# Optimization experiments

Measured on AMD Instinct MI355X. Metric: run time of the kernel, lower is better.

The kernel has to match this reference:

```python
import jax, jax.numpy as jnp
import numpy as np

B, T, IN, H, OUT = 16384, 60, 1, 50, 1


def setup_inputs() -> dict:
    key = jax.random.key(0)
    ks = jax.random.split(key, 7)
    s = 1.0 / np.sqrt(H)
    return {
        "input_seq": jax.random.normal(ks[0], (B, T, IN), dtype=jnp.float32),
        "w_ih": jax.random.uniform(ks[1], (4 * H, IN), jnp.float32, -s, s),
        "w_hh": jax.random.uniform(ks[2], (4 * H, H), jnp.float32, -s, s),
        "b_ih": jax.random.uniform(ks[3], (4 * H,), jnp.float32, -s, s),
        "b_hh": jax.random.uniform(ks[4], (4 * H,), jnp.float32, -s, s),
        "w_lin": jax.random.uniform(ks[5], (OUT, H * T), jnp.float32, -s, s),
        "b_lin": jax.random.uniform(ks[6], (OUT,), jnp.float32, -s, s),
    }


def reference(input_seq, w_ih, w_hh, b_ih, b_hh, w_lin, b_lin):
    # Precompute input projections for all timesteps: [T, B, 4H]
    x_proj = jnp.einsum('bti,gi->tbg', input_seq, w_ih) + b_ih + b_hh

    def step(carry, xp):
        h, c = carry
        gates = xp + h @ w_hh.T  # [B, 4H]
        i, f, g, o = jnp.split(gates, 4, axis=-1)  # PyTorch gate order
        i, f, o = jax.nn.sigmoid(i), jax.nn.sigmoid(f), jax.nn.sigmoid(o)
        g = jnp.tanh(g)
        c = f * c + i * g
        h = o * jnp.tanh(c)
        return (h, c), h

    h0 = jnp.zeros((input_seq.shape[0], H), dtype=input_seq.dtype)
    (_, _), hs = jax.lax.scan(step, (h0, h0), x_proj)  # hs: [T, B, H]
    lstm_out = jnp.transpose(hs, (1, 0, 2)).reshape(-1, H * T)  # [B, T*H]
    return lstm_out @ w_lin.T + b_lin
```

## Files before the change

### kernel.cpp

```cpp
#include <hip/hip_runtime.h>


namespace {
constexpr int TS = 60;

typedef _Float16 half8 __attribute__((ext_vector_type(8)));
typedef _Float16 half2v __attribute__((ext_vector_type(2)));
typedef float f32x4 __attribute__((ext_vector_type(4)));

__device__ __forceinline__ float fexp2(float x) { return __builtin_amdgcn_exp2f(x); }
__device__ __forceinline__ float frcp(float x) { return __builtin_amdgcn_rcpf(x); }
__device__ __forceinline__ f32x4 mfma16(half8 a, half8 b, f32x4 c) {
  return __builtin_amdgcn_mfma_f32_16x16x32_f16(a, b, c, 0, 0, 0);
}
}

__global__ __launch_bounds__(64, 1) void lstm_wv(
    const float* __restrict__ x,
    const float* __restrict__ w_ih,
    const float* __restrict__ w_hh,
    const float* __restrict__ b_ih,
    const float* __restrict__ b_hh,
    const float* __restrict__ w_lin,
    const float* __restrict__ b_lin,
    float* __restrict__ out)
{
  __shared__ unsigned HB[2][16 * 32];
  __shared__ float WLT[4 * 13 * 60];
  __shared__ float XL[TS * 16];

  const int lane = threadIdx.x;
  const int g = lane >> 4;
  const int cl = lane & 15;
  const int s8 = cl & 7;
  const long bbase = (long)blockIdx.x * 16;

  for (int i = lane; i < TS * 16; i += 64) {
    const int b = i / TS, t = i - b * TS;
    XL[t * 16 + b] = x[bbase * TS + i];
  }
  for (int i = lane; i < 4 * 13 * TS; i += 64) {
    const int gg = i / (13 * TS), rem = i - gg * (13 * TS);
    const int T = rem / TS, t = rem - T * TS;
    const int u = 4 * T + gg;
    WLT[i] = (u < 50) ? w_lin[t * 50 + u] : 0.0f;
  }
  for (int i = lane; i < 1024; i += 64) ((unsigned*)HB)[i] = 0u;

  half8 A[13][2];
  {
    const int gate = cl & 3, ur = cl >> 2;
#pragma unroll
    for (int T = 0; T < 13; ++T) {
      const int uA = 4 * T + ur;
      const int orig = gate * 50 + uA;
      const bool valid = (uA < 50);
#pragma unroll
      for (int kc = 0; kc < 2; ++kc) {
        half8 frag;
#pragma unroll
        for (int e = 0; e < 8; ++e) {
          const int k = kc * 32 + 8 * g + e;
          const int j = k >> 3, s = (k >> 1) & 3, cb = k & 1;
          float v = 0.0f;
          if (valid) {
            if (j <= 6) {
              const int u = 8 * j + 4 * cb + s;
              if (u < 50) v = w_hh[orig * 50 + u];
            } else if (k == 62) {
              v = b_ih[orig] + b_hh[orig];
            } else if (k == 63) {
              v = w_ih[orig];
            }
          }
          frag[e] = (_Float16)v;
        }
        A[T][kc] = frag;
      }
    }
  }

  asm volatile("s_waitcnt lgkmcnt(0)" ::: "memory");
  __builtin_amdgcn_sched_barrier(0);

  const int rowb = cl * 32;
  const int clg = rowb + g;
  if (g == 3) {
    const half2v sp = {(_Float16)1.0f, (_Float16)XL[cl]};
    HB[0][clg + ((7 ^ s8) << 2)] = __builtin_bit_cast(unsigned, sp);
  }

  const unsigned b0off = rowb + ((g ^ s8) << 2);
  const unsigned b1off = rowb + (((4 | g) ^ s8) << 2);
  const float* wlb = &WLT[g * 13 * TS];

  float c[13];
#pragma unroll
  for (int T = 0; T < 13; ++T) c[T] = 0.0f;
  float oacc = 0.0f;

  constexpr float L1 = 1.4426950408889634f;
  constexpr float L2 = 2.8853901817779268f;

#pragma unroll 1
  for (int t = 0; t < TS; ++t) {
    const unsigned* HR = HB[t & 1];
    unsigned* HW = HB[(t & 1) ^ 1];
    const half8 B0 = *(const half8*)&HR[b0off];
    const half8 B1 = *(const half8*)&HR[b1off];

    f32x4 d[13];
#pragma unroll
    for (int T = 0; T < 13; ++T) {
      f32x4 a = {0.f, 0.f, 0.f, 0.f};
      a = mfma16(A[T][0], B0, a);
      a = mfma16(A[T][1], B1, a);
      d[T] = a;
    }

    _Float16 hh[14];
    hh[13] = (_Float16)0.0f;
#pragma unroll
    for (int T = 0; T < 13; ++T) {
      const float E1 = fexp2(-L1 * d[T][0]);
      const float E2 = fexp2(-L1 * d[T][1]);
      const float E3 = fexp2(-L1 * d[T][3]);
      const float E4 = fexp2(L2 * d[T][2]);
      const float P1 = 1.0f + E1, P2 = 1.0f + E2;
      const float P3 = 1.0f + E3, P4 = 1.0f + E4;
      const float p12 = P1 * P2, p34 = P3 * P4;
      const float r = frcp(p12 * p34);
      const float r12 = r * p34, r34 = r * p12;
      const float si = r12 * P2, sf = r12 * P1;
      const float so = r34 * P4;
      const float tg = fmaf(-2.0f, r34 * P3, 1.0f);
      const float cn = fmaf(sf, c[T], si * tg);
      c[T] = cn;
      const float Ec = fexp2(L2 * cn);
      const float tc = fmaf(-2.0f, frcp(1.0f + Ec), 1.0f);
      const float hn = so * tc;
      oacc = fmaf(hn, wlb[T * TS + t], oacc);
      hh[T] = (_Float16)hn;
    }

#pragma unroll
    for (int j = 0; j < 7; ++j) {
      const half2v hp = {hh[2 * j], hh[2 * j + 1]};
      HW[clg + ((j ^ s8) << 2)] = __builtin_bit_cast(unsigned, hp);
    }
    if (g == 3) {
      const int tn = (t + 1 < TS) ? (t + 1) : (TS - 1);
      const half2v sp = {(_Float16)1.0f, (_Float16)XL[tn * 16 + cl]};
      HW[clg + ((7 ^ s8) << 2)] = __builtin_bit_cast(unsigned, sp);
    }
    asm volatile("s_waitcnt lgkmcnt(0)" ::: "memory");
    __builtin_amdgcn_sched_barrier(0);
  }

  oacc += __shfl_xor(oacc, 32);
  oacc += __shfl_xor(oacc, 16);
  if (lane < 16) out[bbase + lane] = oacc + b_lin[0];
}

extern "C" void kernel_launch(void* const* d_in, const int* in_sizes, int n_in,
                              void* d_out, int out_size, void* d_ws, size_t ws_size,
                              hipStream_t stream) {
  const float* x     = (const float*)d_in[0];
  const float* w_ih  = (const float*)d_in[1];
  const float* w_hh  = (const float*)d_in[2];
  const float* b_ih  = (const float*)d_in[3];
  const float* b_hh  = (const float*)d_in[4];
  const float* w_lin = (const float*)d_in[5];
  const float* b_lin = (const float*)d_in[6];
  float* out = (float*)d_out;

  dim3 grid(16384 / 16);
  dim3 block(64);
  lstm_wv<<<grid, block, 0, stream>>>(x, w_ih, w_hh, b_ih, b_hh, w_lin,
                                      b_lin, out);
}
```

Measured before the change: 108.1 us.

## Split LSTM hidden units across 8 waves per block with shared h exchange

Replaces the one-wave-per-16-sequences design with 512-thread blocks in which 8 waves each own 2 hidden-unit tiles. Each block handles 32 sequences as two groups. The h state is exchanged through LDS with a __syncthreads every timestep, and partial outputs are reduced across waves at the end. This shortens the serial per-timestep chain for each wave (4 MFMA tiles instead of 13) and raises occupancy, at the cost of a block-wide barrier per step and fewer blocks in the grid. The hidden-unit mapping and the LDS swizzle were redone to match. The L2 constant was also slightly altered, which looks like a typo.

```diff
diff --git a/kernel.cpp b/kernel.cpp
--- a/kernel.cpp
+++ b/kernel.cpp
@@ -7,6 +7,7 @@
 typedef _Float16 half8 __attribute__((ext_vector_type(8)));
 typedef _Float16 half2v __attribute__((ext_vector_type(2)));
 typedef float f32x4 __attribute__((ext_vector_type(4)));
+typedef float f32x2 __attribute__((ext_vector_type(2)));
 
 __device__ __forceinline__ float fexp2(float x) { return __builtin_amdgcn_exp2f(x); }
 __device__ __forceinline__ float frcp(float x) { return __builtin_amdgcn_rcpf(x); }
@@ -15,7 +16,7 @@
 }
 }
 
-__global__ __launch_bounds__(64, 1) void lstm_wv(
+__global__ __launch_bounds__(512, 4) void lstm_w8x2(
     const float* __restrict__ x,
     const float* __restrict__ w_ih,
     const float* __restrict__ w_hh,
@@ -25,34 +26,36 @@
     const float* __restrict__ b_lin,
     float* __restrict__ out)
 {
-  __shared__ unsigned HB[2][16 * 32];
-  __shared__ float WLT[4 * 13 * 60];
-  __shared__ float XL[TS * 16];
+  __shared__ unsigned Hs[2][2][512];
+  __shared__ float WL[TS * 64];
+  __shared__ float XL[TS * 32];
+  __shared__ float OB[8][2][16];
 
-  const int lane = threadIdx.x;
+  const int tid = threadIdx.x;
+  const int lane = tid & 63;
+  const int wv = tid >> 6;
   const int g = lane >> 4;
   const int cl = lane & 15;
   const int s8 = cl & 7;
-  const long bbase = (long)blockIdx.x * 16;
+  const long bbase = (long)blockIdx.x * 32;
 
-  for (int i = lane; i < TS * 16; i += 64) {
+  for (int i = tid; i < TS * 32; i += 512) {
     const int b = i / TS, t = i - b * TS;
-    XL[t * 16 + b] = x[bbase * TS + i];
+    XL[t * 32 + b] = x[bbase * TS + i];
   }
-  for (int i = lane; i < 4 * 13 * TS; i += 64) {
-    const int gg = i / (13 * TS), rem = i - gg * (13 * TS);
-    const int T = rem / TS, t = rem - T * TS;
-    const int u = 4 * T + gg;
-    WLT[i] = (u < 50) ? w_lin[t * 50 + u] : 0.0f;
+  for (int i = tid; i < TS * 64; i += 512) {
+    const int t = i >> 6, u = i & 63;
+    WL[i] = (u < 50) ? w_lin[t * 50 + u] : 0.0f;
   }
-  for (int i = lane; i < 1024; i += 64) ((unsigned*)HB)[i] = 0u;
+  for (int i = tid; i < 2048; i += 512) ((unsigned*)Hs)[i] = 0u;
 
-  half8 A[13][2];
+  half8 A[2][2];
   {
     const int gate = cl & 3, ur = cl >> 2;
 #pragma unroll
-    for (int T = 0; T < 13; ++T) {
-      const int uA = 4 * T + ur;
+    for (int tau = 0; tau < 2; ++tau) {
+      const int T = 2 * wv + tau;
+      const int uA = 16 * ur + T;
       const int orig = gate * 50 + uA;
       const bool valid = (uA < 50);
 #pragma unroll
@@ -61,105 +64,119 @@
 #pragma unroll
         for (int e = 0; e < 8; ++e) {
           const int k = kc * 32 + 8 * g + e;
-          const int j = k >> 3, s = (k >> 1) & 3, cb = k & 1;
           float v = 0.0f;
           if (valid) {
-            if (j <= 6) {
-              const int u = 8 * j + 4 * cb + s;
-              if (u < 50) v = w_hh[orig * 50 + u];
-            } else if (k == 62) {
-              v = b_ih[orig] + b_hh[orig];
-            } else if (k == 63) {
-              v = w_ih[orig];
-            }
+            if (k < 50) v = w_hh[orig * 50 + k];
+            else if (k == 62) v = b_ih[orig] + b_hh[orig];
+            else if (k == 63) v = w_ih[orig];
           }
           frag[e] = (_Float16)v;
         }
-        A[T][kc] = frag;
+        A[tau][kc] = frag;
       }
     }
   }
+  __syncthreads();
 
-  asm volatile("s_waitcnt lgkmcnt(0)" ::: "memory");
-  __builtin_amdgcn_sched_barrier(0);
+  if (wv == 7 && g == 3) {
+#pragma unroll
+    for (int grp = 0; grp < 2; ++grp) {
+      const half2v sp = {(_Float16)1.0f, (_Float16)XL[grp * 16 + cl]};
+      Hs[grp][0][cl * 32 + (((7 ^ s8) << 2) | 3)] =
+          __builtin_bit_cast(unsigned, sp);
+    }
+  }
+  __syncthreads();
 
-  const int rowb = cl * 32;
-  const int clg = rowb + g;
-  if (g == 3) {
-    const half2v sp = {(_Float16)1.0f, (_Float16)XL[cl]};
-    HB[0][clg + ((7 ^ s8) << 2)] = __builtin_bit_cast(unsigned, sp);
-  }
+  const int rowdw = cl * 32;
+  const int rd0 = rowdw + ((g ^ s8) << 2);
+  const int rd1 = rowdw + (((4 | g) ^ s8) << 2);
+  const int hw = 16 * g + 2 * wv;
+  const int wd = rowdw + ((((hw >> 3) ^ s8) << 2) | ((hw & 7) >> 1));
 
-  const unsigned b0off = rowb + ((g ^ s8) << 2);
-  const unsigned b1off = rowb + (((4 | g) ^ s8) << 2);
-  const float* wlb = &WLT[g * 13 * TS];
-
-  float c[13];
-#pragma unroll
-  for (int T = 0; T < 13; ++T) c[T] = 0.0f;
-  float oacc = 0.0f;
+  float c[2][2] = {{0.f, 0.f}, {0.f, 0.f}};
+  float oacc[2] = {0.f, 0.f};
 
   constexpr float L1 = 1.4426950408889634f;
-  constexpr float L2 = 2.8853901817779268f;
+  constexpr float L2 = 2.8853900817779268f;
 
 #pragma unroll 1
   for (int t = 0; t < TS; ++t) {
-    const unsigned* HR = HB[t & 1];
-    unsigned* HW = HB[(t & 1) ^ 1];
-    const half8 B0 = *(const half8*)&HR[b0off];
-    const half8 B1 = *(const half8*)&HR[b1off];
+    const int p = t & 1;
+    half8 B0[2], B1[2];
+#pragma unroll
+    for (int grp = 0; grp < 2; ++grp) {
+      B0[grp] = *(const half8*)&Hs[grp][p][rd0];
+      B1[grp] = *(const half8*)&Hs[grp][p][rd1];
+    }
+    f32x4 d[2][2];
+#pragma unroll
+    for (int grp = 0; grp < 2; ++grp) {
+#pragma unroll
+      for (int tau = 0; tau < 2; ++tau) {
+        f32x4 a = {0.f, 0.f, 0.f, 0.f};
+        a = mfma16(A[tau][0], B0[grp], a);
+        a = mfma16(A[tau][1], B1[grp], a);
+        d[grp][tau] = a;
+      }
+    }
+    const f32x2 wl = *(const f32x2*)&WL[t * 64 + hw];
 
-    f32x4 d[13];
+    half2v hh[2];
 #pragma unroll
-    for (int T = 0; T < 13; ++T) {
-      f32x4 a = {0.f, 0.f, 0.f, 0.f};
-      a = mfma16(A[T][0], B0, a);
-      a = mfma16(A[T][1], B1, a);
-      d[T] = a;
+    for (int grp = 0; grp < 2; ++grp) {
+#pragma unroll
+      for (int tau = 0; tau < 2; ++tau) {
+        const float E1 = fexp2(-L1 * d[grp][tau][0]);
+        const float E2 = fexp2(-L1 * d[grp][tau][1]);
+        const float E3 = fexp2(-L1 * d[grp][tau][3]);
+        const float E4 = fexp2(L2 * d[grp][tau][2]);
+        const float P1 = 1.0f + E1, P2 = 1.0f + E2;
+        const float P3 = 1.0f + E3, P4 = 1.0f + E4;
+        const float p12 = P1 * P2, p34 = P3 * P4;
+        const float r = frcp(p12 * p34);
+        const float r12 = r * p34, r34 = r * p12;
+        const float si = r12 * P2, sf = r12 * P1;
+        const float so = r34 * P4;
+        const float tg = fmaf(-2.0f, r34 * P3, 1.0f);
+        const float cn = fmaf(sf, c[grp][tau], si * tg);
+        c[grp][tau] = cn;
+        const float Ec = fexp2(L2 * cn);
+        const float tc = fmaf(-2.0f, frcp(1.0f + Ec), 1.0f);
+        const float hn = so * tc;
+        oacc[grp] = fmaf(hn, wl[tau], oacc[grp]);
+        hh[grp][tau] = (_Float16)hn;
+      }
     }
 
-    _Float16 hh[14];
-    hh[13] = (_Float16)0.0f;
-#pragma unroll
-    for (int T = 0; T < 13; ++T) {
-      const float E1 = fexp2(-L1 * d[T][0]);
-      const float E2 = fexp2(-L1 * d[T][1]);
-      const float E3 = fexp2(-L1 * d[T][3]);
-      const float E4 = fexp2(L2 * d[T][2]);
-      const float P1 = 1.0f + E1, P2 = 1.0f + E2;
-      const float P3 = 1.0f + E3, P4 = 1.0f + E4;
-      const float p12 = P1 * P2, p34 = P3 * P4;
-      const float r = frcp(p12 * p34);
-      const float r12 = r * p34, r34 = r * p12;
-      const float si = r12 * P2, sf = r12 * P1;
-      const float so = r34 * P4;
-      const float tg = fmaf(-2.0f, r34 * P3, 1.0f);
-      const float cn = fmaf(sf, c[T], si * tg);
-      c[T] = cn;
-      const float Ec = fexp2(L2 * cn);
-      const float tc = fmaf(-2.0f, frcp(1.0f + Ec), 1.0f);
-      const float hn = so * tc;
-      oacc = fmaf(hn, wlb[T * TS + t], oacc);
-      hh[T] = (_Float16)hn;
+    if (wv == 7 && g == 3) {
+      const int tn = (t + 1 < TS) ? (t + 1) : (TS - 1);
+      hh[0][0] = (_Float16)1.0f;
+      hh[0][1] = (_Float16)XL[tn * 32 + cl];
+      hh[1][0] = (_Float16)1.0f;
+      hh[1][1] = (_Float16)XL[tn * 32 + 16 + cl];
     }
-
-#pragma unroll
-    for (int j = 0; j < 7; ++j) {
-      const half2v hp = {hh[2 * j], hh[2 * j + 1]};
-      HW[clg + ((j ^ s8) << 2)] = __builtin_bit_cast(unsigned, hp);
-    }
-    if (g == 3) {
-      const int tn = (t + 1 < TS) ? (t + 1) : (TS - 1);
-      const half2v sp = {(_Float16)1.0f, (_Float16)XL[tn * 16 + cl]};
-      HW[clg + ((7 ^ s8) << 2)] = __builtin_bit_cast(unsigned, sp);
-    }
-    asm volatile("s_waitcnt lgkmcnt(0)" ::: "memory");
-    __builtin_amdgcn_sched_barrier(0);
+    Hs[0][p ^ 1][wd] = __builtin_bit_cast(unsigned, hh[0]);
+    Hs[1][p ^ 1][wd] = __builtin_bit_cast(unsigned, hh[1]);
+    __syncthreads();
   }
 
-  oacc += __shfl_xor(oacc, 32);
-  oacc += __shfl_xor(oacc, 16);
-  if (lane < 16) out[bbase + lane] = oacc + b_lin[0];
+  oacc[0] += __shfl_xor(oacc[0], 32);
+  oacc[0] += __shfl_xor(oacc[0], 16);
+  oacc[1] += __shfl_xor(oacc[1], 32);
+  oacc[1] += __shfl_xor(oacc[1], 16);
+  if (lane < 16) {
+    OB[wv][0][cl] = oacc[0];
+    OB[wv][1][cl] = oacc[1];
+  }
+  __syncthreads();
+  if (tid < 32) {
+    const int grp = tid >> 4, b = tid & 15;
+    float s = b_lin[0];
+#pragma unroll
+    for (int q = 0; q < 8; ++q) s += OB[q][grp][b];
+    out[bbase + grp * 16 + b] = s;
+  }
 }
 
 extern "C" void kernel_launch(void* const* d_in, const int* in_sizes, int n_in,
@@ -174,8 +191,8 @@
   const float* b_lin = (const float*)d_in[6];
   float* out = (float*)d_out;
 
-  dim3 grid(16384 / 16);
-  dim3 block(64);
-  lstm_wv<<<grid, block, 0, stream>>>(x, w_ih, w_hh, b_ih, b_hh, w_lin,
-                                      b_lin, out);
+  dim3 grid(16384 / 32);
+  dim3 block(512);
+  lstm_w8x2<<<grid, block, 0, stream>>>(x, w_ih, w_hh, b_ih, b_hh, w_lin,
+                                        b_lin, out);
 }
```

After: 99.78 us. 1.08x faster.

## Keep LSTM hidden state in registers by remapping gate rows to MFMA layout

Applied to the files above, without the earlier changes.

Reorders the weight-fragment row mapping so that the MFMA output layout of h directly matches the B-operand layout for the next timestep. This removes the per-step LDS write/read double buffer and its wait. The output projection weights are restaged per timestep and read with vector loads. In exchange, the padding grows from 13 to 16 tiles, adding MFMA and transcendental work per step, and a constant was slightly altered.

```diff
diff --git a/kernel.cpp b/kernel.cpp
--- a/kernel.cpp
+++ b/kernel.cpp
@@ -5,7 +5,6 @@
 constexpr int TS = 60;
 
 typedef _Float16 half8 __attribute__((ext_vector_type(8)));
-typedef _Float16 half2v __attribute__((ext_vector_type(2)));
 typedef float f32x4 __attribute__((ext_vector_type(4)));
 
 __device__ __forceinline__ float fexp2(float x) { return __builtin_amdgcn_exp2f(x); }
@@ -15,7 +14,7 @@
 }
 }
 
-__global__ __launch_bounds__(64, 1) void lstm_wv(
+__global__ __launch_bounds__(64, 1) void lstm_reg(
     const float* __restrict__ x,
     const float* __restrict__ w_ih,
     const float* __restrict__ w_hh,
@@ -25,136 +24,121 @@
     const float* __restrict__ b_lin,
     float* __restrict__ out)
 {
-  __shared__ unsigned HB[2][16 * 32];
-  __shared__ float WLT[4 * 13 * 60];
+  __shared__ float WL[TS * 64];
   __shared__ float XL[TS * 16];
 
   const int lane = threadIdx.x;
   const int g = lane >> 4;
   const int cl = lane & 15;
-  const int s8 = cl & 7;
   const long bbase = (long)blockIdx.x * 16;
 
   for (int i = lane; i < TS * 16; i += 64) {
     const int b = i / TS, t = i - b * TS;
     XL[t * 16 + b] = x[bbase * TS + i];
   }
-  for (int i = lane; i < 4 * 13 * TS; i += 64) {
-    const int gg = i / (13 * TS), rem = i - gg * (13 * TS);
-    const int T = rem / TS, t = rem - T * TS;
-    const int u = 4 * T + gg;
-    WLT[i] = (u < 50) ? w_lin[t * 50 + u] : 0.0f;
+  for (int i = lane; i < TS * 64; i += 64) {
+    const int t = i >> 6, u = i & 63;
+    WL[i] = (u < 50) ? w_lin[t * 50 + u] : 0.0f;
   }
-  for (int i = lane; i < 1024; i += 64) ((unsigned*)HB)[i] = 0u;
 
-  half8 A[13][2];
+  half8 A[16][2];
   {
-    const int gate = cl & 3, ur = cl >> 2;
+    const int gateA = cl & 3, urA = cl >> 2;
 #pragma unroll
-    for (int T = 0; T < 13; ++T) {
-      const int uA = 4 * T + ur;
-      const int orig = gate * 50 + uA;
+    for (int T = 0; T < 16; ++T) {
+      const int uA = 8 * urA + (T & 7) + 32 * (T >> 3);
+      const int orig = gateA * 50 + uA;
       const bool valid = (uA < 50);
 #pragma unroll
       for (int kc = 0; kc < 2; ++kc) {
-        half8 frag;
+        half8 fr;
 #pragma unroll
         for (int e = 0; e < 8; ++e) {
           const int k = kc * 32 + 8 * g + e;
-          const int j = k >> 3, s = (k >> 1) & 3, cb = k & 1;
           float v = 0.0f;
           if (valid) {
-            if (j <= 6) {
-              const int u = 8 * j + 4 * cb + s;
-              if (u < 50) v = w_hh[orig * 50 + u];
-            } else if (k == 62) {
-              v = b_ih[orig] + b_hh[orig];
-            } else if (k == 63) {
-              v = w_ih[orig];
-            }
+            if (k < 50) v = w_hh[orig * 50 + k];
+            else if (k == 62) v = b_ih[orig] + b_hh[orig];
+            else if (k == 63) v = w_ih[orig];
           }
-          frag[e] = (_Float16)v;
+          fr[e] = (_Float16)v;
         }
-        A[T][kc] = frag;
+        A[T][kc] = fr;
       }
     }
   }
+  __syncthreads();
 
-  asm volatile("s_waitcnt lgkmcnt(0)" ::: "memory");
-  __builtin_amdgcn_sched_barrier(0);
-
-  const int rowb = cl * 32;
-  const int clg = rowb + g;
+  half8 B0 = {};
+  half8 B1 = {};
   if (g == 3) {
-    const half2v sp = {(_Float16)1.0f, (_Float16)XL[cl]};
-    HB[0][clg + ((7 ^ s8) << 2)] = __builtin_bit_cast(unsigned, sp);
+    B1[6] = (_Float16)1.0f;
+    B1[7] = (_Float16)XL[cl];
   }
 
-  const unsigned b0off = rowb + ((g ^ s8) << 2);
-  const unsigned b1off = rowb + (((4 | g) ^ s8) << 2);
-  const float* wlb = &WLT[g * 13 * TS];
-
-  float c[13];
+  float c[16];
 #pragma unroll
-  for (int T = 0; T < 13; ++T) c[T] = 0.0f;
+  for (int T = 0; T < 16; ++T) c[T] = 0.0f;
   float oacc = 0.0f;
 
   constexpr float L1 = 1.4426950408889634f;
-  constexpr float L2 = 2.8853901817779268f;
+  constexpr float L2 = 2.8853900817779268f;
 
 #pragma unroll 1
   for (int t = 0; t < TS; ++t) {
-    const unsigned* HR = HB[t & 1];
-    unsigned* HW = HB[(t & 1) ^ 1];
-    const half8 B0 = *(const half8*)&HR[b0off];
-    const half8 B1 = *(const half8*)&HR[b1off];
-
-    f32x4 d[13];
+    f32x4 acc[16];
 #pragma unroll
-    for (int T = 0; T < 13; ++T) {
+    for (int T = 0; T < 16; ++T) {
       f32x4 a = {0.f, 0.f, 0.f, 0.f};
       a = mfma16(A[T][0], B0, a);
       a = mfma16(A[T][1], B1, a);
-      d[T] = a;
+      acc[T] = a;
     }
+    const f32x4 wla = *(const f32x4*)&WL[t * 64 + 8 * g];
+    const f32x4 wlb = *(const f32x4*)&WL[t * 64 + 8 * g + 4];
+    const f32x4 wlc = *(const f32x4*)&WL[t * 64 + 32 + 8 * g];
+    const f32x4 wld = *(const f32x4*)&WL[t * 64 + 32 + 8 * g + 4];
+    const int tn = (t + 1 < TS) ? (t + 1) : (TS - 1);
+    const float xnext = XL[tn * 16 + cl];
 
-    _Float16 hh[14];
-    hh[13] = (_Float16)0.0f;
+    _Float16 hh[16];
 #pragma unroll
-    for (int T = 0; T < 13; ++T) {
-      const float E1 = fexp2(-L1 * d[T][0]);
-      const float E2 = fexp2(-L1 * d[T][1]);
-      const float E3 = fexp2(-L1 * d[T][3]);
-      const float E4 = fexp2(L2 * d[T][2]);
+    for (int T = 0; T < 16; ++T) {
+      const float E1 = fexp2(-L1 * acc[T][0]);
+      const float E2 = fexp2(-L1 * acc[T][1]);
+      const float E3 = fexp2(-L1 * acc[T][3]);
+      const float E4 = fexp2(L2 * acc[T][2]);
       const float P1 = 1.0f + E1, P2 = 1.0f + E2;
       const float P3 = 1.0f + E3, P4 = 1.0f + E4;
       const float p12 = P1 * P2, p34 = P3 * P4;
       const float r = frcp(p12 * p34);
       const float r12 = r * p34, r34 = r * p12;
-      const float si = r12 * P2, sf = r12 * P1;
-      const float so = r34 * P4;
+      const float si = r12 * P2, sf = r12 * P1, so = r34 * P4;
       const float tg = fmaf(-2.0f, r34 * P3, 1.0f);
       const float cn = fmaf(sf, c[T], si * tg);
       c[T] = cn;
       const float Ec = fexp2(L2 * cn);
       const float tc = fmaf(-2.0f, frcp(1.0f + Ec), 1.0f);
       const float hn = so * tc;
-      oacc = fmaf(hn, wlb[T * TS + t], oacc);
+      const float wv = (T < 4) ? wla[T]
+                     : (T < 8) ? wlb[T - 4]
+                     : (T < 12) ? wlc[T - 8] : wld[T - 12];
+      oacc = fmaf(hn, wv, oacc);
       hh[T] = (_Float16)hn;
     }
 
+    half8 nB0, nB1;
 #pragma unroll
-    for (int j = 0; j < 7; ++j) {
-      const half2v hp = {hh[2 * j], hh[2 * j + 1]};
-      HW[clg + ((j ^ s8) << 2)] = __builtin_bit_cast(unsigned, hp);
+    for (int e = 0; e < 8; ++e) {
+      nB0[e] = hh[e];
+      nB1[e] = hh[8 + e];
     }
     if (g == 3) {
-      const int tn = (t + 1 < TS) ? (t + 1) : (TS - 1);
-      const half2v sp = {(_Float16)1.0f, (_Float16)XL[tn * 16 + cl]};
-      HW[clg + ((7 ^ s8) << 2)] = __builtin_bit_cast(unsigned, sp);
+      nB1[6] = (_Float16)1.0f;
+      nB1[7] = (_Float16)xnext;
     }
-    asm volatile("s_waitcnt lgkmcnt(0)" ::: "memory");
-    __builtin_amdgcn_sched_barrier(0);
+    B0 = nB0;
+    B1 = nB1;
   }
 
   oacc += __shfl_xor(oacc, 32);
@@ -176,6 +160,6 @@
 
   dim3 grid(16384 / 16);
   dim3 block(64);
-  lstm_wv<<<grid, block, 0, stream>>>(x, w_ih, w_hh, b_ih, b_hh, w_lin,
-                                      b_lin, out);
+  lstm_reg<<<grid, block, 0, stream>>>(x, w_ih, w_hh, b_ih, b_hh, w_lin,
+                                       b_lin, out);
 }
```

Result: slower. 112.1 us (+3.7%).
